# Kernel tuning notes

Measured on AMD Instinct MI355X. Metric: run time of the kernel, lower is better.

## Reference

```python
import jax, jax.numpy as jnp
import numpy as np

E, N, D, H = 500000, 100000, 128, 128
LN_EPS = 1e-5


def setup_inputs() -> dict:
    key = jax.random.key(0)
    ks = jax.random.split(key, 8)
    efeat = jax.random.normal(ks[0], (E, D), dtype=jnp.float32)
    nfeat = jax.random.normal(ks[1], (N, D), dtype=jnp.float32)
    src = jax.random.randint(ks[2], (E,), 0, N, dtype=jnp.int64)
    dst = jax.random.randint(ks[3], (E,), 0, N, dtype=jnp.int64)
    dim_cat = 2 * D + D  # 2*input_dim_nodes + input_dim_edges = 384
    w1 = jax.random.normal(ks[4], (dim_cat, H), dtype=jnp.float32) / np.sqrt(dim_cat)
    b1 = jnp.zeros((H,), dtype=jnp.float32)
    w2 = jax.random.normal(ks[5], (H, D), dtype=jnp.float32) / np.sqrt(H)
    b2 = jnp.zeros((D,), dtype=jnp.float32)
    gamma = jnp.ones((D,), dtype=jnp.float32)
    beta = jnp.zeros((D,), dtype=jnp.float32)
    return {"efeat": efeat, "nfeat": nfeat, "src": src, "dst": dst,
            "w1": w1, "b1": b1, "w2": w2, "b2": b2, "gamma": gamma, "beta": beta}


def reference(efeat, nfeat, src, dst, w1, b1, w2, b2, gamma, beta):
    # gather per-edge src/dst node features and concat with edge features: [E, 2D+D]
    cat_feat = jnp.concatenate([efeat, nfeat[src], nfeat[dst]], axis=-1)
    # MeshGraphMLP with hidden_layers=1: Linear -> SiLU -> Linear -> LayerNorm
    h = jax.nn.silu(cat_feat @ w1 + b1)          # [E, H]
    y = h @ w2 + b2                               # [E, D]
    mu = jnp.mean(y, axis=-1, keepdims=True)
    var = jnp.mean((y - mu) ** 2, axis=-1, keepdims=True)
    y = (y - mu) * jax.lax.rsqrt(var + LN_EPS) * gamma + beta
    efeat_new = y + efeat                         # residual add
    return (efeat_new, nfeat)
```

## Files before the change

### kernel.cpp

```cpp
#include <hip/hip_runtime.h>

#define E_CONST 500000
#define N_CONST 100000

typedef __attribute__((ext_vector_type(8))) short bf16x8;
typedef __attribute__((ext_vector_type(4))) float f32x4;
typedef __attribute__((ext_vector_type(4))) unsigned u32x4;

__global__ __launch_bounds__(256) void prep_weights(const float* __restrict__ w1,
                                                    const float* __restrict__ w2,
                                                    short* __restrict__ ws) {
    int idx  = blockIdx.x * 256 + threadIdx.x;
    int frag = idx >> 9;
    int r    = idx & 511;
    int lane = r >> 3, j = r & 7;
    const float* w;
    int fi;
    if (frag < 96) { w = w1; fi = frag; }
    else           { w = w2; fi = frag - 96; }
    int kk = fi >> 3, nn = fi & 7;
    int k = kk * 32 + (lane >> 4) * 8 + j;
    int n = nn * 16 + (lane & 15);
    unsigned u = __float_as_uint(w[k * 128 + n]);
    u = u + 0x7FFFu + ((u >> 16) & 1u);
    ws[idx] = (short)(u >> 16);
}

__global__ __launch_bounds__(256) void copy_nfeat(const float* __restrict__ nfeat,
                                                  float* __restrict__ out) {
    size_t idx = (size_t)(blockIdx.x * 256 + threadIdx.x) * 4;
    *(f32x4*)(out + idx) = *(const f32x4*)(nfeat + idx);
}

__device__ __forceinline__ unsigned pack_bf16_trunc(float lo, float hi) {
    return __builtin_amdgcn_perm(__float_as_uint(hi), __float_as_uint(lo), 0x07060302u);
}

__global__ __launch_bounds__(256, 2) void edge_mlp(
    const float* __restrict__ efeat, const float* __restrict__ nfeat,
    const int* __restrict__ src, const int* __restrict__ dst,
    const short* __restrict__ wsw,
    const float* __restrict__ b1, const float* __restrict__ b2,
    const float* __restrict__ gamma, const float* __restrict__ beta,
    float* __restrict__ out) {

    __shared__ short hs[64 * 136];
    __shared__ float ys[64 * 132];
    __shared__ float mu_s[64];
    __shared__ float rs_s[64];

    const int tid   = threadIdx.x;
    const int lane  = tid & 63;
    const int nw    = tid >> 6;
    const int l15   = lane & 15;
    const int quad  = lane >> 4;
    const int eBase = blockIdx.x * 64;

    bf16x8 b1f[2][12];
    bf16x8 b2f[2][4];
#pragma unroll
    for (int t = 0; t < 2; ++t) {
        int nn = nw * 2 + t;
#pragma unroll
        for (int kk = 0; kk < 12; ++kk)
            b1f[t][kk] = *(const bf16x8*)(wsw + ((kk * 8 + nn) * 64 + lane) * 8);
#pragma unroll
        for (int kk = 0; kk < 4; ++kk)
            b2f[t][kk] = *(const bf16x8*)(wsw + 49152 + ((kk * 8 + nn) * 64 + lane) * 8);
    }
    const float bb1[2] = { b1[nw * 32 + l15], b1[nw * 32 + 16 + l15] };
    const float bb2[2] = { b2[nw * 32 + l15], b2[nw * 32 + 16 + l15] };

#pragma unroll 1
    for (int mt = 0; mt < 4; ++mt) {
        int e = eBase + mt * 16 + l15;
        if (e >= E_CONST) e = E_CONST - 1;
        int s = src[e], d = dst[e];
        const float* pe = efeat + (size_t)e * 128 + quad * 8;
        const float* ps = nfeat + (size_t)s * 128 + quad * 8;
        const float* pd = nfeat + (size_t)d * 128 + quad * 8;

        f32x4 acc0 = {0.f, 0.f, 0.f, 0.f}, acc1 = {0.f, 0.f, 0.f, 0.f};
#pragma unroll
        for (int kk = 0; kk < 12; ++kk) {
            const float* p = (kk < 4) ? (pe + kk * 32)
                           : (kk < 8) ? (ps + (kk - 4) * 32)
                                      : (pd + (kk - 8) * 32);
            f32x4 f0 = *(const f32x4*)p;
            f32x4 f1 = *(const f32x4*)(p + 4);
            u32x4 pk;
            pk.x = pack_bf16_trunc(f0.x, f0.y);
            pk.y = pack_bf16_trunc(f0.z, f0.w);
            pk.z = pack_bf16_trunc(f1.x, f1.y);
            pk.w = pack_bf16_trunc(f1.z, f1.w);
            bf16x8 a = __builtin_bit_cast(bf16x8, pk);
            acc0 = __builtin_amdgcn_mfma_f32_16x16x32_bf16(a, b1f[0][kk], acc0, 0, 0, 0);
            acc1 = __builtin_amdgcn_mfma_f32_16x16x32_bf16(a, b1f[1][kk], acc1, 0, 0, 0);
        }
#pragma unroll
        for (int t = 0; t < 2; ++t) {
            f32x4 acc = (t == 0) ? acc0 : acc1;
            int col = nw * 32 + t * 16 + l15;
#pragma unroll
            for (int i = 0; i < 4; ++i) {
                float x  = acc[i] + bb1[t];
                float sg = __builtin_amdgcn_rcpf(1.0f + __expf(-x));
                float h  = x * sg;
                int row  = mt * 16 + quad * 4 + i;
                unsigned u = __float_as_uint(h);
                u = u + 0x7FFFu + ((u >> 16) & 1u);
                hs[row * 136 + col] = (short)(u >> 16);
            }
        }
    }
    __syncthreads();

#pragma unroll 1
    for (int mt = 0; mt < 4; ++mt) {
        int arow = mt * 16 + l15;
        f32x4 acc0 = {0.f, 0.f, 0.f, 0.f}, acc1 = {0.f, 0.f, 0.f, 0.f};
#pragma unroll
        for (int kk = 0; kk < 4; ++kk) {
            bf16x8 a = *(const bf16x8*)(hs + arow * 136 + kk * 32 + quad * 8);
            acc0 = __builtin_amdgcn_mfma_f32_16x16x32_bf16(a, b2f[0][kk], acc0, 0, 0, 0);
            acc1 = __builtin_amdgcn_mfma_f32_16x16x32_bf16(a, b2f[1][kk], acc1, 0, 0, 0);
        }
#pragma unroll
        for (int t = 0; t < 2; ++t) {
            f32x4 acc = (t == 0) ? acc0 : acc1;
            int col = nw * 32 + t * 16 + l15;
#pragma unroll
            for (int i = 0; i < 4; ++i)
                ys[(mt * 16 + quad * 4 + i) * 132 + col] = acc[i] + bb2[t];
        }
    }
    __syncthreads();

    {
        int row = tid >> 2;
        int part = tid & 3;
        const float* yr = ys + row * 132 + part * 32;
        float sum = 0.f, sq = 0.f;
#pragma unroll
        for (int k = 0; k < 8; ++k) {
            f32x4 v = *(const f32x4*)(yr + k * 4);
            sum += v.x + v.y + v.z + v.w;
            sq  += v.x * v.x + v.y * v.y + v.z * v.z + v.w * v.w;
        }
        sum += __shfl_xor(sum, 1); sq += __shfl_xor(sq, 1);
        sum += __shfl_xor(sum, 2); sq += __shfl_xor(sq, 2);
        if (part == 0) {
            float mu  = sum * (1.0f / 128.0f);
            float var = sq * (1.0f / 128.0f) - mu * mu;
            mu_s[row] = mu;
            rs_s[row] = __builtin_amdgcn_rsqf(var + 1e-5f);
        }
    }
    __syncthreads();

    {
        int c4 = tid & 31;
        f32x4 g4  = *(const f32x4*)(gamma + c4 * 4);
        f32x4 bt4 = *(const f32x4*)(beta  + c4 * 4);
#pragma unroll 1
        for (int it = 0; it < 8; ++it) {
            int row = it * 8 + (tid >> 5);
            int e = eBase + row;
            if (e < E_CONST) {
                float mu = mu_s[row], rs = rs_s[row];
                f32x4 y  = *(const f32x4*)(ys + row * 132 + c4 * 4);
                f32x4 ef = *(const f32x4*)(efeat + (size_t)e * 128 + c4 * 4);
                f32x4 o;
                o.x = (y.x - mu) * rs * g4.x + bt4.x + ef.x;
                o.y = (y.y - mu) * rs * g4.y + bt4.y + ef.y;
                o.z = (y.z - mu) * rs * g4.z + bt4.z + ef.z;
                o.w = (y.w - mu) * rs * g4.w + bt4.w + ef.w;
                *(f32x4*)(out + (size_t)e * 128 + c4 * 4) = o;
            }
        }
    }
}

extern "C" void kernel_launch(void* const* d_in, const int* in_sizes, int n_in,
                              void* d_out, int out_size, void* d_ws, size_t ws_size,
                              hipStream_t stream) {
    const float* efeat = (const float*)d_in[0];
    const float* nfeat = (const float*)d_in[1];
    const int*   src   = (const int*)d_in[2];
    const int*   dst   = (const int*)d_in[3];
    const float* w1    = (const float*)d_in[4];
    const float* b1    = (const float*)d_in[5];
    const float* w2    = (const float*)d_in[6];
    const float* b2    = (const float*)d_in[7];
    const float* gamma = (const float*)d_in[8];
    const float* beta  = (const float*)d_in[9];
    float* out = (float*)d_out;
    short* wsw = (short*)d_ws;

    hipLaunchKernelGGL(prep_weights, dim3(256), dim3(256), 0, stream, w1, w2, wsw);
    hipLaunchKernelGGL(copy_nfeat, dim3(12500), dim3(256), 0, stream,
                       nfeat, out + (size_t)E_CONST * 128);
    hipLaunchKernelGGL(edge_mlp, dim3((E_CONST + 63) / 64), dim3(256), 0, stream,
                       efeat, nfeat, src, dst, wsw, b1, b2, gamma, beta, out);
}
```

Before: 842.6 us.

## Stage gathered node rows in LDS and fuse LayerNorm on register accumulators

The src and dst node rows are now gathered cooperatively into shared memory as bf16, using contiguous per-thread loads, instead of each lane doing strided gathers inside the MFMA loop. The second-GEMM results stay in registers. LayerNorm statistics are reduced with wave shuffles plus a small shared partial-sum buffer, which removes the ys staging buffer and one pass over it. The trade-off is more shared memory per block (a 64x264 bf16 tile), which may lower occupancy. The final output stores become scalar 4-byte writes spread across columns rather than 16-byte vectors, which may weaken store coalescing.

```diff
diff --git a/kernel.cpp b/kernel.cpp
--- a/kernel.cpp
+++ b/kernel.cpp
@@ -36,6 +36,15 @@
     return __builtin_amdgcn_perm(__float_as_uint(hi), __float_as_uint(lo), 0x07060302u);
 }
 
+__device__ __forceinline__ bf16x8 pack8(f32x4 f0, f32x4 f1) {
+    u32x4 pk;
+    pk.x = pack_bf16_trunc(f0.x, f0.y);
+    pk.y = pack_bf16_trunc(f0.z, f0.w);
+    pk.z = pack_bf16_trunc(f1.x, f1.y);
+    pk.w = pack_bf16_trunc(f1.z, f1.w);
+    return __builtin_bit_cast(bf16x8, pk);
+}
+
 __global__ __launch_bounds__(256, 2) void edge_mlp(
     const float* __restrict__ efeat, const float* __restrict__ nfeat,
     const int* __restrict__ src, const int* __restrict__ dst,
@@ -44,8 +53,10 @@
     const float* __restrict__ gamma, const float* __restrict__ beta,
     float* __restrict__ out) {
 
+    __shared__ short As[64 * 264];
     __shared__ short hs[64 * 136];
-    __shared__ float ys[64 * 132];
+    __shared__ float psum_s[256];
+    __shared__ float psq_s[256];
     __shared__ float mu_s[64];
     __shared__ float rs_s[64];
 
@@ -70,30 +81,45 @@
     }
     const float bb1[2] = { b1[nw * 32 + l15], b1[nw * 32 + 16 + l15] };
     const float bb2[2] = { b2[nw * 32 + l15], b2[nw * 32 + 16 + l15] };
+    const float gg[2]  = { gamma[nw * 32 + l15], gamma[nw * 32 + 16 + l15] };
+    const float bt[2]  = { beta[nw * 32 + l15],  beta[nw * 32 + 16 + l15] };
+
+    {
+        int r  = tid >> 1;
+        int hf = tid & 1;
+        int e  = eBase + (r & 63);
+        if (e >= E_CONST) e = E_CONST - 1;
+        int idx = (r < 64) ? src[e] : dst[e];
+        const float* p = nfeat + (size_t)idx * 128 + hf * 64;
+        short* wp = As + (r & 63) * 264 + (r >> 6) * 128 + hf * 64;
+#pragma unroll 4
+        for (int j = 0; j < 8; ++j) {
+            f32x4 f0 = *(const f32x4*)(p + j * 8);
+            f32x4 f1 = *(const f32x4*)(p + j * 8 + 4);
+            *(bf16x8*)(wp + j * 8) = pack8(f0, f1);
+        }
+    }
+    __syncthreads();
 
 #pragma unroll 1
     for (int mt = 0; mt < 4; ++mt) {
         int e = eBase + mt * 16 + l15;
         if (e >= E_CONST) e = E_CONST - 1;
-        int s = src[e], d = dst[e];
         const float* pe = efeat + (size_t)e * 128 + quad * 8;
-        const float* ps = nfeat + (size_t)s * 128 + quad * 8;
-        const float* pd = nfeat + (size_t)d * 128 + quad * 8;
+        const short* ap = As + (mt * 16 + l15) * 264 + quad * 8;
 
         f32x4 acc0 = {0.f, 0.f, 0.f, 0.f}, acc1 = {0.f, 0.f, 0.f, 0.f};
 #pragma unroll
-        for (int kk = 0; kk < 12; ++kk) {
-            const float* p = (kk < 4) ? (pe + kk * 32)
-                           : (kk < 8) ? (ps + (kk - 4) * 32)
-                                      : (pd + (kk - 8) * 32);
-            f32x4 f0 = *(const f32x4*)p;
-            f32x4 f1 = *(const f32x4*)(p + 4);
-            u32x4 pk;
-            pk.x = pack_bf16_trunc(f0.x, f0.y);
-            pk.y = pack_bf16_trunc(f0.z, f0.w);
-            pk.z = pack_bf16_trunc(f1.x, f1.y);
-            pk.w = pack_bf16_trunc(f1.z, f1.w);
-            bf16x8 a = __builtin_bit_cast(bf16x8, pk);
+        for (int kk = 0; kk < 4; ++kk) {
+            f32x4 f0 = *(const f32x4*)(pe + kk * 32);
+            f32x4 f1 = *(const f32x4*)(pe + kk * 32 + 4);
+            bf16x8 a = pack8(f0, f1);
+            acc0 = __builtin_amdgcn_mfma_f32_16x16x32_bf16(a, b1f[0][kk], acc0, 0, 0, 0);
+            acc1 = __builtin_amdgcn_mfma_f32_16x16x32_bf16(a, b1f[1][kk], acc1, 0, 0, 0);
+        }
+#pragma unroll
+        for (int kk = 4; kk < 12; ++kk) {
+            bf16x8 a = *(const bf16x8*)(ap + (kk - 4) * 32);
             acc0 = __builtin_amdgcn_mfma_f32_16x16x32_bf16(a, b1f[0][kk], acc0, 0, 0, 0);
             acc1 = __builtin_amdgcn_mfma_f32_16x16x32_bf16(a, b1f[1][kk], acc1, 0, 0, 0);
         }
@@ -115,7 +141,8 @@
     }
     __syncthreads();
 
-#pragma unroll 1
+    f32x4 y0[4], y1[4];
+#pragma unroll
     for (int mt = 0; mt < 4; ++mt) {
         int arow = mt * 16 + l15;
         f32x4 acc0 = {0.f, 0.f, 0.f, 0.f}, acc1 = {0.f, 0.f, 0.f, 0.f};
@@ -125,57 +152,55 @@
             acc0 = __builtin_amdgcn_mfma_f32_16x16x32_bf16(a, b2f[0][kk], acc0, 0, 0, 0);
             acc1 = __builtin_amdgcn_mfma_f32_16x16x32_bf16(a, b2f[1][kk], acc1, 0, 0, 0);
         }
-#pragma unroll
-        for (int t = 0; t < 2; ++t) {
-            f32x4 acc = (t == 0) ? acc0 : acc1;
-            int col = nw * 32 + t * 16 + l15;
-#pragma unroll
-            for (int i = 0; i < 4; ++i)
-                ys[(mt * 16 + quad * 4 + i) * 132 + col] = acc[i] + bb2[t];
-        }
-    }
-    __syncthreads();
-
-    {
-        int row = tid >> 2;
-        int part = tid & 3;
-        const float* yr = ys + row * 132 + part * 32;
-        float sum = 0.f, sq = 0.f;
-#pragma unroll
-        for (int k = 0; k < 8; ++k) {
-            f32x4 v = *(const f32x4*)(yr + k * 4);
-            sum += v.x + v.y + v.z + v.w;
-            sq  += v.x * v.x + v.y * v.y + v.z * v.z + v.w * v.w;
-        }
-        sum += __shfl_xor(sum, 1); sq += __shfl_xor(sq, 1);
-        sum += __shfl_xor(sum, 2); sq += __shfl_xor(sq, 2);
-        if (part == 0) {
-            float mu  = sum * (1.0f / 128.0f);
-            float var = sq * (1.0f / 128.0f) - mu * mu;
-            mu_s[row] = mu;
-            rs_s[row] = __builtin_amdgcn_rsqf(var + 1e-5f);
-        }
-    }
-    __syncthreads();
-
-    {
-        int c4 = tid & 31;
-        f32x4 g4  = *(const f32x4*)(gamma + c4 * 4);
-        f32x4 bt4 = *(const f32x4*)(beta  + c4 * 4);
-#pragma unroll 1
-        for (int it = 0; it < 8; ++it) {
-            int row = it * 8 + (tid >> 5);
+        f32x4 bv0 = { bb2[0], bb2[0], bb2[0], bb2[0] };
+        f32x4 bv1 = { bb2[1], bb2[1], bb2[1], bb2[1] };
+        y0[mt] = acc0 + bv0;
+        y1[mt] = acc1 + bv1;
+    }
+
+#pragma unroll
+    for (int mt = 0; mt < 4; ++mt) {
+#pragma unroll
+        for (int i = 0; i < 4; ++i) {
+            float a0 = y0[mt][i], a1 = y1[mt][i];
+            float s = a0 + a1;
+            float q = a0 * a0 + a1 * a1;
+            s += __shfl_xor(s, 1);  q += __shfl_xor(q, 1);
+            s += __shfl_xor(s, 2);  q += __shfl_xor(q, 2);
+            s += __shfl_xor(s, 4);  q += __shfl_xor(q, 4);
+            s += __shfl_xor(s, 8);  q += __shfl_xor(q, 8);
+            if (l15 == 0) {
+                int row = mt * 16 + quad * 4 + i;
+                psum_s[row * 4 + nw] = s;
+                psq_s [row * 4 + nw] = q;
+            }
+        }
+    }
+    __syncthreads();
+
+    if (tid < 64) {
+        f32x4 ps = *(const f32x4*)(psum_s + tid * 4);
+        f32x4 pq = *(const f32x4*)(psq_s  + tid * 4);
+        float mu = (ps.x + ps.y + ps.z + ps.w) * (1.0f / 128.0f);
+        float m2 = (pq.x + pq.y + pq.z + pq.w) * (1.0f / 128.0f);
+        mu_s[tid] = mu;
+        rs_s[tid] = __builtin_amdgcn_rsqf(m2 - mu * mu + 1e-5f);
+    }
+    __syncthreads();
+
+#pragma unroll
+    for (int mt = 0; mt < 4; ++mt) {
+#pragma unroll
+        for (int i = 0; i < 4; ++i) {
+            int row = mt * 16 + quad * 4 + i;
             int e = eBase + row;
             if (e < E_CONST) {
                 float mu = mu_s[row], rs = rs_s[row];
-                f32x4 y  = *(const f32x4*)(ys + row * 132 + c4 * 4);
-                f32x4 ef = *(const f32x4*)(efeat + (size_t)e * 128 + c4 * 4);
-                f32x4 o;
-                o.x = (y.x - mu) * rs * g4.x + bt4.x + ef.x;
-                o.y = (y.y - mu) * rs * g4.y + bt4.y + ef.y;
-                o.z = (y.z - mu) * rs * g4.z + bt4.z + ef.z;
-                o.w = (y.w - mu) * rs * g4.w + bt4.w + ef.w;
-                *(f32x4*)(out + (size_t)e * 128 + c4 * 4) = o;
+                int col0 = nw * 32 + l15;
+                const float* pef = efeat + (size_t)e * 128;
+                float* po = out + (size_t)e * 128;
+                po[col0]      = (y0[mt][i] - mu) * rs * gg[0] + bt[0] + pef[col0];
+                po[col0 + 16] = (y1[mt][i] - mu) * rs * gg[1] + bt[1] + pef[col0 + 16];
             }
         }
     }
```

Result: faster. 749.1 us (-11.1%).
